# Optimization experiments

Measured on AMD Instinct MI355X. Metric: run time of the kernel, lower is better.

## Reference

```python
import jax, jax.numpy as jnp
import numpy as np

NUM_HEADS = 16
HEAD_DIM = 64
D_DEC = 1024
D_ENC = 1024
R = 256  # kv_lora_rank
LN_EPS = 1e-5


def setup_inputs() -> dict:
    key = jax.random.key(0)
    ks = jax.random.split(key, 8)
    B, SQ, SK = 4, 2048, 4096
    query = jax.random.normal(ks[0], (B, SQ, D_DEC), dtype=jnp.float32)
    encoder_output = jax.random.normal(ks[1], (B, SK, D_ENC), dtype=jnp.float32)
    s = 0.02
    Wq = jax.random.normal(ks[2], (NUM_HEADS * HEAD_DIM, D_DEC), dtype=jnp.float32) * s
    Wkva = jax.random.normal(ks[3], (R, D_ENC), dtype=jnp.float32) * s
    ln_g = jnp.ones((R,), dtype=jnp.float32)
    ln_b = jnp.zeros((R,), dtype=jnp.float32)
    Wkvb = jax.random.normal(ks[4], (NUM_HEADS * 2 * HEAD_DIM, R), dtype=jnp.float32) * s
    Wout = jax.random.normal(ks[5], (D_DEC, NUM_HEADS * HEAD_DIM), dtype=jnp.float32) * s
    return {"query": query, "encoder_output": encoder_output, "Wq": Wq,
            "Wkva": Wkva, "ln_g": ln_g, "ln_b": ln_b, "Wkvb": Wkvb, "Wout": Wout}


def reference(query, encoder_output, Wq, Wkva, ln_g, ln_b, Wkvb, Wout):
    B, SQ, _ = query.shape
    SK = encoder_output.shape[1]
    H, Dh = NUM_HEADS, HEAD_DIM

    # q projection -> [B, H, SQ, Dh]
    q = jnp.einsum('bsd,ed->bse', query, Wq).reshape(B, SQ, H, Dh).transpose(0, 2, 1, 3)

    # low-rank KV compression + layernorm
    c = jnp.einsum('bsd,rd->bsr', encoder_output, Wkva)  # [B, SK, R]
    mu = jnp.mean(c, axis=-1, keepdims=True)
    var = jnp.mean(jnp.square(c - mu), axis=-1, keepdims=True)
    c = (c - mu) * jax.lax.rsqrt(var + LN_EPS) * ln_g + ln_b

    # decompress to K,V: [B, SK, H, 2*Dh] -> split
    kv = jnp.einsum('bsr,er->bse', c, Wkvb).reshape(B, SK, H, 2 * Dh).transpose(0, 2, 1, 3)
    k, v = kv[..., :Dh], kv[..., Dh:]

    scale = 1.0 / np.sqrt(Dh).astype(np.float32)
    scores = jnp.einsum('bhqd,bhkd->bhqk', q, k) * scale
    attn = jax.nn.softmax(scores, axis=-1)  # dropout is identity in eval / p=0
    o = jnp.einsum('bhqk,bhkd->bhqd', attn, v)
    o = o.transpose(0, 2, 1, 3).reshape(B, SQ, H * Dh)
    return jnp.einsum('bse,de->bsd', o, Wout)
```

## Files before the change

kernel.cpp:

```cpp
#include <hip/hip_runtime.h>

#define LOG2E 1.4426950408889634f

typedef __attribute__((ext_vector_type(8))) short short8;
typedef __attribute__((ext_vector_type(4))) float f32x4;

__device__ inline unsigned short f2bf(float f) {
  unsigned u = __float_as_uint(f);
  u += 0x7fffu + ((u >> 16) & 1u);
  return (unsigned short)(u >> 16);
}

#define MFMA16(a, b, c) __builtin_amdgcn_mfma_f32_16x16x32_bf16((a), (b), (c), 0, 0, 0)

#define GLDS16(gp, lp)                                                              \
  __builtin_amdgcn_global_load_lds((const __attribute__((address_space(1))) void*)(gp), \
                                   (__attribute__((address_space(3))) void*)(lp), 16, 0, 0)

__device__ inline f32x4 zero4() {
  f32x4 z = {0.f, 0.f, 0.f, 0.f};
  return z;
}

__device__ inline int swz8(int row) { return (row ^ (row >> 3)) & 7; }

__global__ __launch_bounds__(256) void k_cast6(
    const float* __restrict__ e, const float* __restrict__ q, const float* __restrict__ wq,
    const float* __restrict__ wo, const float* __restrict__ wb, const float* __restrict__ wa,
    unsigned short* __restrict__ eo, unsigned short* __restrict__ qo, unsigned short* __restrict__ wqo,
    unsigned short* __restrict__ woo, unsigned short* __restrict__ wbo, unsigned short* __restrict__ wao) {
  int i = (blockIdx.x * 256 + threadIdx.x) * 4;
  const float* src;
  unsigned short* dst;
  int off;
  if (i < 16777216) { src = e; dst = eo; off = i; }
  else if (i < 25165824) { src = q; dst = qo; off = i - 16777216; }
  else if (i < 26214400) { src = wq; dst = wqo; off = i - 25165824; }
  else if (i < 27262976) { src = wo; dst = woo; off = i - 26214400; }
  else if (i < 27787264) { src = wb; dst = wbo; off = i - 27262976; }
  else { src = wa; dst = wao; off = i - 27787264; }
  float4 v = *(const float4*)(src + off);
  unsigned lo = (unsigned)f2bf(v.x) | ((unsigned)f2bf(v.y) << 16);
  unsigned hi = (unsigned)f2bf(v.z) | ((unsigned)f2bf(v.w) << 16);
  *(uint2*)(dst + off) = make_uint2(lo, hi);
}

__global__ __launch_bounds__(256, 2) void k_qproj(const unsigned short* __restrict__ A,
                                                  const unsigned short* __restrict__ Bw,
                                                  unsigned short* __restrict__ Qout) {
  __shared__ __align__(16) short As[128 * 32];
  __shared__ __align__(16) short Bs[128 * 32];
  const int K = 1024;
  int tid = threadIdx.x;
  int w = tid >> 6, lane = tid & 63, quad = lane >> 4, c = lane & 15;
  int m0 = blockIdx.x * 128, n0 = blockIdx.y * 128;
  int wm = (w >> 1) * 64, wn = (w & 1) * 64;
  f32x4 acc[4][4];
#pragma unroll
  for (int i = 0; i < 4; i++)
#pragma unroll
    for (int j = 0; j < 4; j++) acc[i][j] = zero4();

  for (int k0 = 0; k0 < K; k0 += 32) {
#pragma unroll
    for (int i = 0; i < 2; i++) {
      int seg = w * 2 + i;
      int bo = seg * 1024 + lane * 16;
      int row = bo >> 6, col = (bo & 63) >> 1;
      GLDS16(A + (size_t)(m0 + row) * K + k0 + col, (char*)As + seg * 1024);
      GLDS16(Bw + (size_t)(n0 + row) * K + k0 + col, (char*)Bs + seg * 1024);
    }
    __syncthreads();
    short8 af[4], bfr[4];
#pragma unroll
    for (int i = 0; i < 4; i++) {
      af[i] = *(const short8*)&As[(wm + i * 16 + c) * 32 + quad * 8];
      bfr[i] = *(const short8*)&Bs[(wn + i * 16 + c) * 32 + quad * 8];
    }
#pragma unroll
    for (int mi = 0; mi < 4; mi++)
#pragma unroll
      for (int ni = 0; ni < 4; ni++) acc[mi][ni] = MFMA16(af[mi], bfr[ni], acc[mi][ni]);
    __syncthreads();
  }
  const float scale = 0.125f * LOG2E;
#pragma unroll
  for (int mi = 0; mi < 4; mi++) {
    int rowb = m0 + wm + mi * 16 + quad * 4;
#pragma unroll
    for (int ni = 0; ni < 4; ni++) {
      int col = n0 + wn + ni * 16 + c;
      int h = col >> 6, d = col & 63;
#pragma unroll
      for (int r = 0; r < 4; r++) {
        int row = rowb + r;
        int b = row >> 11, sq = row & 2047;
        Qout[(((size_t)(b * 16 + h)) * 2048 + sq) * 64 + d] = f2bf(acc[mi][ni][r] * scale);
      }
    }
  }
}

__global__ __launch_bounds__(256, 2) void k_cln(const unsigned short* __restrict__ E,
                                                const unsigned short* __restrict__ Wa,
                                                const float* __restrict__ g, const float* __restrict__ bb,
                                                unsigned short* __restrict__ Cout) {
  __shared__ __align__(16) short As[64 * 32];
  __shared__ __align__(16) short Bs[256 * 32];
  __shared__ float redS[4][64], redQ[4][64];
  __shared__ float gS[256], bS[256];
  const int K = 1024;
  int tid = threadIdx.x;
  int w = tid >> 6, lane = tid & 63, quad = lane >> 4, c = lane & 15;
  int m0 = blockIdx.x * 64;
  gS[tid] = g[tid];
  bS[tid] = bb[tid];
  f32x4 acc[4][4];
#pragma unroll
  for (int i = 0; i < 4; i++)
#pragma unroll
    for (int j = 0; j < 4; j++) acc[i][j] = zero4();

  for (int k0 = 0; k0 < K; k0 += 32) {
    {
      int bo = w * 1024 + lane * 16;
      int row = bo >> 6, col = (bo & 63) >> 1;
      GLDS16(E + (size_t)(m0 + row) * K + k0 + col, (char*)As + w * 1024);
    }
#pragma unroll
    for (int i = 0; i < 4; i++) {
      int seg = w * 4 + i;
      int bo = seg * 1024 + lane * 16;
      int row = bo >> 6, col = (bo & 63) >> 1;
      GLDS16(Wa + (size_t)row * K + k0 + col, (char*)Bs + seg * 1024);
    }
    __syncthreads();
    short8 af[4], bfr[4];
#pragma unroll
    for (int i = 0; i < 4; i++) {
      af[i] = *(const short8*)&As[(i * 16 + c) * 32 + quad * 8];
      bfr[i] = *(const short8*)&Bs[(w * 64 + i * 16 + c) * 32 + quad * 8];
    }
#pragma unroll
    for (int mi = 0; mi < 4; mi++)
#pragma unroll
      for (int ni = 0; ni < 4; ni++) acc[mi][ni] = MFMA16(af[mi], bfr[ni], acc[mi][ni]);
    __syncthreads();
  }
  float ps[4][4], pq[4][4];
#pragma unroll
  for (int mi = 0; mi < 4; mi++)
#pragma unroll
    for (int r = 0; r < 4; r++) {
      float s = 0.f, q = 0.f;
#pragma unroll
      for (int ni = 0; ni < 4; ni++) {
        float x = acc[mi][ni][r];
        s += x;
        q += x * x;
      }
      for (int m = 1; m < 16; m <<= 1) {
        s += __shfl_xor(s, m, 64);
        q += __shfl_xor(q, m, 64);
      }
      ps[mi][r] = s;
      pq[mi][r] = q;
    }
  if (c == 0) {
#pragma unroll
    for (int mi = 0; mi < 4; mi++)
#pragma unroll
      for (int r = 0; r < 4; r++) {
        int row = mi * 16 + quad * 4 + r;
        redS[w][row] = ps[mi][r];
        redQ[w][row] = pq[mi][r];
      }
  }
  __syncthreads();
  float muv[4][4], rsv[4][4];
#pragma unroll
  for (int mi = 0; mi < 4; mi++)
#pragma unroll
    for (int r = 0; r < 4; r++) {
      int row = mi * 16 + quad * 4 + r;
      float S = redS[0][row] + redS[1][row] + redS[2][row] + redS[3][row];
      float Q = redQ[0][row] + redQ[1][row] + redQ[2][row] + redQ[3][row];
      float mu = S * (1.f / 256.f);
      float var = Q * (1.f / 256.f) - mu * mu;
      muv[mi][r] = mu;
      rsv[mi][r] = rsqrtf(var + 1e-5f);
    }
#pragma unroll
  for (int mi = 0; mi < 4; mi++)
#pragma unroll
    for (int ni = 0; ni < 4; ni++) {
      int col = w * 64 + ni * 16 + c;
#pragma unroll
      for (int r = 0; r < 4; r++) {
        int row = m0 + mi * 16 + quad * 4 + r;
        float y = (acc[mi][ni][r] - muv[mi][r]) * rsv[mi][r] * gS[col] + bS[col];
        Cout[(size_t)row * 256 + col] = f2bf(y);
      }
    }
}

__global__ __launch_bounds__(256, 2) void k_kv(const unsigned short* __restrict__ A,
                                               const unsigned short* __restrict__ Bw,
                                               unsigned short* __restrict__ Kb,
                                               unsigned short* __restrict__ Vb) {
  __shared__ __align__(16) short As[128 * 32];
  __shared__ __align__(16) short Bs[128 * 32];
  const int K = 256;
  int tid = threadIdx.x;
  int w = tid >> 6, lane = tid & 63, quad = lane >> 4, c = lane & 15;
  int m0 = blockIdx.x * 128, n0 = blockIdx.y * 128;
  int wm = (w >> 1) * 64, wn = (w & 1) * 64;
  f32x4 acc[4][4];
#pragma unroll
  for (int i = 0; i < 4; i++)
#pragma unroll
    for (int j = 0; j < 4; j++) acc[i][j] = zero4();

  for (int k0 = 0; k0 < K; k0 += 32) {
#pragma unroll
    for (int i = 0; i < 2; i++) {
      int seg = w * 2 + i;
      int bo = seg * 1024 + lane * 16;
      int row = bo >> 6, col = (bo & 63) >> 1;
      GLDS16(A + (size_t)(m0 + row) * K + k0 + col, (char*)As + seg * 1024);
      GLDS16(Bw + (size_t)(n0 + row) * K + k0 + col, (char*)Bs + seg * 1024);
    }
    __syncthreads();
    short8 af[4], bfr[4];
#pragma unroll
    for (int i = 0; i < 4; i++) {
      af[i] = *(const short8*)&As[(wm + i * 16 + c) * 32 + quad * 8];
      bfr[i] = *(const short8*)&Bs[(wn + i * 16 + c) * 32 + quad * 8];
    }
#pragma unroll
    for (int mi = 0; mi < 4; mi++)
#pragma unroll
      for (int ni = 0; ni < 4; ni++) acc[mi][ni] = MFMA16(af[mi], bfr[ni], acc[mi][ni]);
    __syncthreads();
  }
#pragma unroll
  for (int mi = 0; mi < 4; mi++) {
    int rowb = m0 + wm + mi * 16 + quad * 4;
#pragma unroll
    for (int ni = 0; ni < 4; ni++) {
      int col = n0 + wn + ni * 16 + c;
      int h = col >> 7, rr = col & 127;
#pragma unroll
      for (int r = 0; r < 4; r++) {
        int row = rowb + r;
        int b = row >> 12, sk = row & 4095;
        float x = acc[mi][ni][r];
        if (rr < 64)
          Kb[(((size_t)(b * 16 + h)) * 4096 + sk) * 64 + rr] = f2bf(x);
        else
          Vb[(((size_t)(b * 16 + h)) * 64 + (rr - 64)) * 4096 + sk] = f2bf(x);
      }
    }
  }
}

__global__ __launch_bounds__(256, 2) void k_attn(const unsigned short* __restrict__ Qb,
                                                 const unsigned short* __restrict__ Kb,
                                                 const unsigned short* __restrict__ Vb,
                                                 unsigned short* __restrict__ Ob) {
  __shared__ __align__(16) short Qs[256 * 64];
  __shared__ __align__(16) short KVs[2][2 * 64 * 64];
  int tid = threadIdx.x;
  int w = tid >> 6, lane = tid & 63, quad = lane >> 4, c = lane & 15;
  int r8 = lane >> 3, pc = lane & 7;
  int bh = blockIdx.y, qt = blockIdx.x;
  const unsigned short* Qp = Qb + ((size_t)bh * 2048 + qt * 256) * 64;
  const unsigned short* Kp = Kb + (size_t)bh * 4096 * 64;
  const unsigned short* Vp = Vb + (size_t)bh * 64 * 4096;

#pragma unroll
  for (int i = 0; i < 8; i++) {
    int seg = w * 8 + i;
    int row = seg * 8 + r8;
    int lc = pc ^ swz8(row);
    GLDS16(Qp + (size_t)row * 64 + lc * 8, (char*)Qs + seg * 1024);
  }
#pragma unroll
  for (int i = 0; i < 4; i++) {
    int seg = w * 4 + i;
    int row = (seg & 7) * 8 + r8;
    int lc = pc ^ swz8(row);
    if (seg < 8)
      GLDS16(Kp + (size_t)row * 64 + lc * 8, (char*)KVs[0] + seg * 1024);
    else
      GLDS16(Vp + (size_t)row * 4096 + lc * 8, (char*)KVs[0] + seg * 1024);
  }
  __syncthreads();
  short8 qf[4][2];
#pragma unroll
  for (int nt = 0; nt < 4; nt++) {
    int row = w * 64 + nt * 16 + c;
#pragma unroll
    for (int kk = 0; kk < 2; kk++)
      qf[nt][kk] = *(const short8*)((const char*)Qs + row * 128 + (((kk * 4 + quad) ^ swz8(row)) << 4));
  }
  char* PsW = (char*)Qs + w * 8192;

  f32x4 O[4][4];
  float lp[4] = {0.f, 0.f, 0.f, 0.f};
#pragma unroll
  for (int i = 0; i < 4; i++)
#pragma unroll
    for (int j = 0; j < 4; j++) O[i][j] = zero4();

  for (int kt = 0; kt < 64; kt++) {
    const char* KsC = (const char*)KVs[kt & 1];
    const char* VsC = KsC + 8192;
    if (kt < 63) {
      char* nb = (char*)KVs[(kt + 1) & 1];
#pragma unroll
      for (int i = 0; i < 4; i++) {
        int seg = w * 4 + i;
        int row = (seg & 7) * 8 + r8;
        int lc = pc ^ swz8(row);
        if (seg < 8)
          GLDS16(Kp + ((size_t)(kt + 1) * 64 + row) * 64 + lc * 8, nb + seg * 1024);
        else
          GLDS16(Vp + (size_t)row * 4096 + (kt + 1) * 64 + lc * 8, nb + seg * 1024);
      }
    }

#pragma unroll
    for (int mt = 0; mt < 4; mt++) {
      int krow = mt * 16 + c;
      short8 kf0 = *(const short8*)(KsC + krow * 128 + ((quad ^ swz8(krow)) << 4));
      short8 kf1 = *(const short8*)(KsC + krow * 128 + (((4 + quad) ^ swz8(krow)) << 4));
      f32x4 s[4];
#pragma unroll
      for (int nt = 0; nt < 4; nt++) {
        s[nt] = MFMA16(kf0, qf[nt][0], zero4());
        s[nt] = MFMA16(kf1, qf[nt][1], s[nt]);
      }
#pragma unroll
      for (int nt = 0; nt < 4; nt++) {
        float p0 = __builtin_amdgcn_exp2f(s[nt][0]);
        float p1 = __builtin_amdgcn_exp2f(s[nt][1]);
        float p2 = __builtin_amdgcn_exp2f(s[nt][2]);
        float p3 = __builtin_amdgcn_exp2f(s[nt][3]);
        lp[nt] += (p0 + p1) + (p2 + p3);
        unsigned u0 = ((__float_as_uint(p0) + 0x8000u) >> 16) | ((__float_as_uint(p1) + 0x8000u) & 0xffff0000u);
        unsigned u1 = ((__float_as_uint(p2) + 0x8000u) >> 16) | ((__float_as_uint(p3) + 0x8000u) & 0xffff0000u);
        int prow = nt * 16 + c;
        int chunk = (mt * 2 + (quad >> 1)) ^ swz8(prow);
        *(uint2*)(PsW + prow * 128 + (chunk << 4) + (quad & 1) * 8) = make_uint2(u0, u1);
      }
    }

#pragma unroll
    for (int kk = 0; kk < 2; kk++) {
      short8 vf[4];
#pragma unroll
      for (int dt = 0; dt < 4; dt++) {
        int vrow = dt * 16 + c;
        vf[dt] = *(const short8*)(VsC + vrow * 128 + (((kk * 4 + quad) ^ swz8(vrow)) << 4));
      }
#pragma unroll
      for (int mo = 0; mo < 4; mo++) {
        int prow = mo * 16 + c;
        short8 pf = *(const short8*)((const char*)PsW + prow * 128 + (((kk * 4 + quad) ^ swz8(prow)) << 4));
#pragma unroll
        for (int dt = 0; dt < 4; dt++) O[mo][dt] = MFMA16(pf, vf[dt], O[mo][dt]);
      }
    }
    __syncthreads();
  }

#pragma unroll
  for (int nt = 0; nt < 4; nt++) {
    lp[nt] += __shfl_xor(lp[nt], 16, 64);
    lp[nt] += __shfl_xor(lp[nt], 32, 64);
  }
  int b = bh >> 4, h = bh & 15;
#pragma unroll
  for (int mo = 0; mo < 4; mo++) {
#pragma unroll
    for (int r = 0; r < 4; r++) {
      float inv = __builtin_amdgcn_rcpf(__shfl(lp[mo], quad * 4 + r, 64));
      int sq = qt * 256 + w * 64 + mo * 16 + quad * 4 + r;
#pragma unroll
      for (int dt = 0; dt < 4; dt++)
        Ob[((size_t)b * 2048 + sq) * 1024 + h * 64 + dt * 16 + c] = f2bf(O[mo][dt][r] * inv);
    }
  }
}

__global__ __launch_bounds__(256, 2) void k_out(const unsigned short* __restrict__ A,
                                                const unsigned short* __restrict__ Bw,
                                                float* __restrict__ Out) {
  __shared__ __align__(16) short As[128 * 32];
  __shared__ __align__(16) short Bs[128 * 32];
  const int K = 1024;
  int tid = threadIdx.x;
  int w = tid >> 6, lane = tid & 63, quad = lane >> 4, c = lane & 15;
  int m0 = blockIdx.x * 128, n0 = blockIdx.y * 128;
  int wm = (w >> 1) * 64, wn = (w & 1) * 64;
  f32x4 acc[4][4];
#pragma unroll
  for (int i = 0; i < 4; i++)
#pragma unroll
    for (int j = 0; j < 4; j++) acc[i][j] = zero4();

  for (int k0 = 0; k0 < K; k0 += 32) {
#pragma unroll
    for (int i = 0; i < 2; i++) {
      int seg = w * 2 + i;
      int bo = seg * 1024 + lane * 16;
      int row = bo >> 6, col = (bo & 63) >> 1;
      GLDS16(A + (size_t)(m0 + row) * K + k0 + col, (char*)As + seg * 1024);
      GLDS16(Bw + (size_t)(n0 + row) * K + k0 + col, (char*)Bs + seg * 1024);
    }
    __syncthreads();
    short8 af[4], bfr[4];
#pragma unroll
    for (int i = 0; i < 4; i++) {
      af[i] = *(const short8*)&As[(wm + i * 16 + c) * 32 + quad * 8];
      bfr[i] = *(const short8*)&Bs[(wn + i * 16 + c) * 32 + quad * 8];
    }
#pragma unroll
    for (int mi = 0; mi < 4; mi++)
#pragma unroll
      for (int ni = 0; ni < 4; ni++) acc[mi][ni] = MFMA16(af[mi], bfr[ni], acc[mi][ni]);
    __syncthreads();
  }
#pragma unroll
  for (int mi = 0; mi < 4; mi++) {
    int rowb = m0 + wm + mi * 16 + quad * 4;
#pragma unroll
    for (int ni = 0; ni < 4; ni++) {
      int col = n0 + wn + ni * 16 + c;
#pragma unroll
      for (int r = 0; r < 4; r++) Out[(size_t)(rowb + r) * 1024 + col] = acc[mi][ni][r];
    }
  }
}

extern "C" void kernel_launch(void* const* d_in, const int* in_sizes, int n_in,
                              void* d_out, int out_size, void* d_ws, size_t ws_size,
                              hipStream_t stream) {
  const float* query = (const float*)d_in[0];
  const float* enc = (const float*)d_in[1];
  const float* Wq = (const float*)d_in[2];
  const float* Wkva = (const float*)d_in[3];
  const float* ln_g = (const float*)d_in[4];
  const float* ln_b = (const float*)d_in[5];
  const float* Wkvb = (const float*)d_in[6];
  const float* Wout = (const float*)d_in[7];
  if (ws_size < 81264640) return;

  char* ws = (char*)d_ws;
  unsigned short* wq_bf = (unsigned short*)(ws + 0);
  unsigned short* wa_bf = (unsigned short*)(ws + 2097152);
  unsigned short* wb_bf = (unsigned short*)(ws + 2621440);
  unsigned short* wo_bf = (unsigned short*)(ws + 3670016);
  unsigned short* qproj = (unsigned short*)(ws + 5767168);
  unsigned short* cln = (unsigned short*)(ws + 22544384);
  unsigned short* ebf_v = (unsigned short*)(ws + 30932992);
  unsigned short* qin_o = (unsigned short*)(ws + 64487424);
  unsigned short* kbuf = (unsigned short*)d_out;

  k_cast6<<<27392, 256, 0, stream>>>(enc, query, Wq, Wout, Wkvb, Wkva,
                                     ebf_v, qin_o, wq_bf, wo_bf, wb_bf, wa_bf);

  k_qproj<<<dim3(64, 8), 256, 0, stream>>>(qin_o, wq_bf, qproj);
  k_cln<<<256, 256, 0, stream>>>(ebf_v, wa_bf, ln_g, ln_b, cln);
  k_kv<<<dim3(128, 16), 256, 0, stream>>>(cln, wb_bf, kbuf, ebf_v);
  k_attn<<<dim3(8, 64), 256, 0, stream>>>(qproj, kbuf, ebf_v, qin_o);
  k_out<<<dim3(64, 8), 256, 0, stream>>>(qin_o, wo_bf, (float*)d_out);
}
```

Baseline: 460.7 us.

## Split attention over key halves with combine kernel and single-buffered LDS

The attention kernel is templated to split the key sequence into NS chunks across a new grid dimension. Each chunk writes unnormalized bf16 partial outputs and row sums, and a new k_comb kernel adds the partials and normalizes them. The split path runs only when the workspace is large enough. Q fragments are now loaded straight from global memory into registers, and KV staging drops to a single LDS buffer with a per-wave P tile, which reduces LDS use so launch bounds can target 4 blocks per CU. The aim is more blocks per CU and more parallelism (1024 blocks instead of 512), at the cost of an extra pass over the output, lost overlap of the next KV load with compute, and extra bf16 rounding of the partials.

```diff
diff --git a/kernel.cpp b/kernel.cpp
--- a/kernel.cpp
+++ b/kernel.cpp
@@ -264,47 +264,56 @@
   }
 }
 
-__global__ __launch_bounds__(256, 2) void k_attn(const unsigned short* __restrict__ Qb,
+template <int NS>
+__global__ __launch_bounds__(256, 4) void k_attn(const unsigned short* __restrict__ Qb,
                                                  const unsigned short* __restrict__ Kb,
                                                  const unsigned short* __restrict__ Vb,
-                                                 unsigned short* __restrict__ Ob) {
-  __shared__ __align__(16) short Qs[256 * 64];
-  __shared__ __align__(16) short KVs[2][2 * 64 * 64];
+                                                 unsigned short* __restrict__ O0,
+                                                 unsigned short* __restrict__ O1,
+                                                 float* __restrict__ l0,
+                                                 float* __restrict__ l1) {
+  __shared__ __align__(16) short KVs[2 * 64 * 64];
+  __shared__ __align__(16) short Ps[4][2048];
   int tid = threadIdx.x;
   int w = tid >> 6, lane = tid & 63, quad = lane >> 4, c = lane & 15;
   int r8 = lane >> 3, pc = lane & 7;
-  int bh = blockIdx.y, qt = blockIdx.x;
-  const unsigned short* Qp = Qb + ((size_t)bh * 2048 + qt * 256) * 64;
-  const unsigned short* Kp = Kb + (size_t)bh * 4096 * 64;
-  const unsigned short* Vp = Vb + (size_t)bh * 64 * 4096;
-
-#pragma unroll
-  for (int i = 0; i < 8; i++) {
-    int seg = w * 8 + i;
-    int row = seg * 8 + r8;
-    int lc = pc ^ swz8(row);
-    GLDS16(Qp + (size_t)row * 64 + lc * 8, (char*)Qs + seg * 1024);
-  }
+  int qt = blockIdx.x, ks = blockIdx.y, bh = blockIdx.z;
+  const int ITERS = 64 / NS;
+
+  const char* Kg = (const char*)Kb + (size_t)bh * 524288 + (size_t)ks * 262144;
+  const char* Vg = (const char*)Vb + (size_t)bh * 524288 + (size_t)ks * 4096;
+  const unsigned short* Qv = Qb + ((size_t)bh * 2048 + qt * 256 + w * 64) * 64 + c * 64 + quad * 8;
+
+  const char* sg[4];
+  int step = (w < 2) ? 8192 : 128;
 #pragma unroll
   for (int i = 0; i < 4; i++) {
     int seg = w * 4 + i;
-    int row = (seg & 7) * 8 + r8;
-    int lc = pc ^ swz8(row);
-    if (seg < 8)
-      GLDS16(Kp + (size_t)row * 64 + lc * 8, (char*)KVs[0] + seg * 1024);
-    else
-      GLDS16(Vp + (size_t)row * 4096 + lc * 8, (char*)KVs[0] + seg * 1024);
-  }
-  __syncthreads();
+    if (w < 2) {
+      int row = seg * 8 + r8;
+      sg[i] = Kg + row * 128 + ((pc ^ r8) << 4);
+    } else {
+      int vrow = (seg - 8) * 8 + r8;
+      sg[i] = Vg + (size_t)vrow * 8192 + ((pc ^ r8) << 4);
+    }
+  }
+
+  int kb0 = c * 128 + ((quad ^ (c & 7)) << 4);
+  int kb1 = c * 128 + (((quad + 4) ^ (c & 7)) << 4);
+  const char* KsB0 = (const char*)KVs + kb0;
+  const char* KsB1 = (const char*)KVs + kb1;
+  const char* VsB0 = (const char*)KVs + 8192 + kb0;
+  const char* VsB1 = (const char*)KVs + 8192 + kb1;
+  int sP = (c >> 1) & 3;
+  char* pw0 = (char*)Ps[w] + c * 64 + (quad & 1) * 8 + (((quad >> 1) ^ sP) << 4);
+  char* pw1 = (char*)Ps[w] + c * 64 + (quad & 1) * 8 + ((((quad >> 1) + 2) ^ sP) << 4);
+  const char* prB = (const char*)Ps[w] + c * 64 + ((quad ^ sP) << 4);
+
   short8 qf[4][2];
 #pragma unroll
-  for (int nt = 0; nt < 4; nt++) {
-    int row = w * 64 + nt * 16 + c;
-#pragma unroll
-    for (int kk = 0; kk < 2; kk++)
-      qf[nt][kk] = *(const short8*)((const char*)Qs + row * 128 + (((kk * 4 + quad) ^ swz8(row)) << 4));
-  }
-  char* PsW = (char*)Qs + w * 8192;
+  for (int nt = 0; nt < 4; nt++)
+#pragma unroll
+    for (int h = 0; h < 2; h++) qf[nt][h] = *(const short8*)(Qv + nt * 1024 + h * 32);
 
   f32x4 O[4][4];
   float lp[4] = {0.f, 0.f, 0.f, 0.f};
@@ -313,66 +322,64 @@
 #pragma unroll
     for (int j = 0; j < 4; j++) O[i][j] = zero4();
 
-  for (int kt = 0; kt < 64; kt++) {
-    const char* KsC = (const char*)KVs[kt & 1];
-    const char* VsC = KsC + 8192;
-    if (kt < 63) {
-      char* nb = (char*)KVs[(kt + 1) & 1];
+#pragma unroll
+  for (int i = 0; i < 4; i++) {
+    GLDS16(sg[i], (char*)KVs + (w * 4 + i) * 1024);
+    sg[i] += step;
+  }
+
+  for (int kt = 0; kt < ITERS; kt++) {
+    __syncthreads();
+#pragma unroll
+    for (int kk = 0; kk < 2; kk++) {
+#pragma unroll
+      for (int mtl = 0; mtl < 2; mtl++) {
+        int mt = kk * 2 + mtl;
+        short8 kf0 = *(const short8*)(KsB0 + mt * 2048);
+        short8 kf1 = *(const short8*)(KsB1 + mt * 2048);
+        f32x4 s[4];
+#pragma unroll
+        for (int nt = 0; nt < 4; nt++) {
+          s[nt] = MFMA16(kf0, qf[nt][0], zero4());
+          s[nt] = MFMA16(kf1, qf[nt][1], s[nt]);
+        }
+#pragma unroll
+        for (int nt = 0; nt < 4; nt++) {
+          float p0 = __builtin_amdgcn_exp2f(s[nt][0]);
+          float p1 = __builtin_amdgcn_exp2f(s[nt][1]);
+          float p2 = __builtin_amdgcn_exp2f(s[nt][2]);
+          float p3 = __builtin_amdgcn_exp2f(s[nt][3]);
+          lp[nt] += (p0 + p1) + (p2 + p3);
+          unsigned r0 = __float_as_uint(p0) + 0x8000u;
+          unsigned r1 = __float_as_uint(p1) + 0x8000u;
+          unsigned r2 = __float_as_uint(p2) + 0x8000u;
+          unsigned r3 = __float_as_uint(p3) + 0x8000u;
+          unsigned lo = __builtin_amdgcn_perm(r1, r0, 0x07060302u);
+          unsigned hi = __builtin_amdgcn_perm(r3, r2, 0x07060302u);
+          *(uint2*)((mtl ? pw1 : pw0) + nt * 1024) = make_uint2(lo, hi);
+        }
+      }
+      {
+        const char* VsB = kk ? VsB1 : VsB0;
+        short8 vf[4];
+#pragma unroll
+        for (int dt = 0; dt < 4; dt++) vf[dt] = *(const short8*)(VsB + dt * 2048);
+#pragma unroll
+        for (int mo = 0; mo < 4; mo++) {
+          short8 pf = *(const short8*)(prB + mo * 1024);
+#pragma unroll
+          for (int dt = 0; dt < 4; dt++) O[mo][dt] = MFMA16(pf, vf[dt], O[mo][dt]);
+        }
+      }
+    }
+    __syncthreads();
+    if (kt + 1 < ITERS) {
 #pragma unroll
       for (int i = 0; i < 4; i++) {
-        int seg = w * 4 + i;
-        int row = (seg & 7) * 8 + r8;
-        int lc = pc ^ swz8(row);
-        if (seg < 8)
-          GLDS16(Kp + ((size_t)(kt + 1) * 64 + row) * 64 + lc * 8, nb + seg * 1024);
-        else
-          GLDS16(Vp + (size_t)row * 4096 + (kt + 1) * 64 + lc * 8, nb + seg * 1024);
-      }
-    }
-
-#pragma unroll
-    for (int mt = 0; mt < 4; mt++) {
-      int krow = mt * 16 + c;
-      short8 kf0 = *(const short8*)(KsC + krow * 128 + ((quad ^ swz8(krow)) << 4));
-      short8 kf1 = *(const short8*)(KsC + krow * 128 + (((4 + quad) ^ swz8(krow)) << 4));
-      f32x4 s[4];
-#pragma unroll
-      for (int nt = 0; nt < 4; nt++) {
-        s[nt] = MFMA16(kf0, qf[nt][0], zero4());
-        s[nt] = MFMA16(kf1, qf[nt][1], s[nt]);
-      }
-#pragma unroll
-      for (int nt = 0; nt < 4; nt++) {
-        float p0 = __builtin_amdgcn_exp2f(s[nt][0]);
-        float p1 = __builtin_amdgcn_exp2f(s[nt][1]);
-        float p2 = __builtin_amdgcn_exp2f(s[nt][2]);
-        float p3 = __builtin_amdgcn_exp2f(s[nt][3]);
-        lp[nt] += (p0 + p1) + (p2 + p3);
-        unsigned u0 = ((__float_as_uint(p0) + 0x8000u) >> 16) | ((__float_as_uint(p1) + 0x8000u) & 0xffff0000u);
-        unsigned u1 = ((__float_as_uint(p2) + 0x8000u) >> 16) | ((__float_as_uint(p3) + 0x8000u) & 0xffff0000u);
-        int prow = nt * 16 + c;
-        int chunk = (mt * 2 + (quad >> 1)) ^ swz8(prow);
-        *(uint2*)(PsW + prow * 128 + (chunk << 4) + (quad & 1) * 8) = make_uint2(u0, u1);
-      }
-    }
-
-#pragma unroll
-    for (int kk = 0; kk < 2; kk++) {
-      short8 vf[4];
-#pragma unroll
-      for (int dt = 0; dt < 4; dt++) {
-        int vrow = dt * 16 + c;
-        vf[dt] = *(const short8*)(VsC + vrow * 128 + (((kk * 4 + quad) ^ swz8(vrow)) << 4));
-      }
-#pragma unroll
-      for (int mo = 0; mo < 4; mo++) {
-        int prow = mo * 16 + c;
-        short8 pf = *(const short8*)((const char*)PsW + prow * 128 + (((kk * 4 + quad) ^ swz8(prow)) << 4));
-#pragma unroll
-        for (int dt = 0; dt < 4; dt++) O[mo][dt] = MFMA16(pf, vf[dt], O[mo][dt]);
-      }
-    }
-    __syncthreads();
+        GLDS16(sg[i], (char*)KVs + (w * 4 + i) * 1024);
+        sg[i] += step;
+      }
+    }
   }
 
 #pragma unroll
@@ -381,17 +388,57 @@
     lp[nt] += __shfl_xor(lp[nt], 32, 64);
   }
   int b = bh >> 4, h = bh & 15;
-#pragma unroll
-  for (int mo = 0; mo < 4; mo++) {
-#pragma unroll
-    for (int r = 0; r < 4; r++) {
-      float inv = __builtin_amdgcn_rcpf(__shfl(lp[mo], quad * 4 + r, 64));
-      int sq = qt * 256 + w * 64 + mo * 16 + quad * 4 + r;
-#pragma unroll
-      for (int dt = 0; dt < 4; dt++)
-        Ob[((size_t)b * 2048 + sq) * 1024 + h * 64 + dt * 16 + c] = f2bf(O[mo][dt][r] * inv);
-    }
-  }
+  if (NS == 1) {
+#pragma unroll
+    for (int mo = 0; mo < 4; mo++) {
+#pragma unroll
+      for (int r = 0; r < 4; r++) {
+        float inv = __builtin_amdgcn_rcpf(__shfl(lp[mo], quad * 4 + r, 64));
+        int sq = qt * 256 + w * 64 + mo * 16 + quad * 4 + r;
+#pragma unroll
+        for (int dt = 0; dt < 4; dt++)
+          O0[((size_t)b * 2048 + sq) * 1024 + h * 64 + dt * 16 + c] = f2bf(O[mo][dt][r] * inv);
+      }
+    }
+  } else {
+    unsigned short* Op = ks ? O1 : O0;
+    float* lq = ks ? l1 : l0;
+#pragma unroll
+    for (int mo = 0; mo < 4; mo++) {
+#pragma unroll
+      for (int r = 0; r < 4; r++) {
+        int sq = qt * 256 + w * 64 + mo * 16 + quad * 4 + r;
+#pragma unroll
+        for (int dt = 0; dt < 4; dt++)
+          Op[((size_t)b * 2048 + sq) * 1024 + h * 64 + dt * 16 + c] = f2bf(O[mo][dt][r]);
+      }
+    }
+    float lsel = lp[0];
+    if (quad == 1) lsel = lp[1];
+    if (quad == 2) lsel = lp[2];
+    if (quad == 3) lsel = lp[3];
+    lq[(size_t)bh * 2048 + qt * 256 + w * 64 + quad * 16 + c] = lsel;
+  }
+}
+
+__global__ __launch_bounds__(256) void k_comb(unsigned short* __restrict__ A,
+                                              const unsigned short* __restrict__ Bp,
+                                              const float* __restrict__ lA,
+                                              const float* __restrict__ lB) {
+  int i = (blockIdx.x * 256 + threadIdx.x) * 4;
+  int row = i >> 10, col = i & 1023;
+  int bh = ((row >> 11) << 4) + (col >> 6);
+  int li = bh * 2048 + (row & 2047);
+  float inv = __builtin_amdgcn_rcpf(lA[li] + lB[li]);
+  uint2 a = *(const uint2*)(A + i);
+  uint2 bb = *(const uint2*)(Bp + i);
+  float o0 = __uint_as_float(a.x << 16) + __uint_as_float(bb.x << 16);
+  float o1 = __uint_as_float(a.x & 0xffff0000u) + __uint_as_float(bb.x & 0xffff0000u);
+  float o2 = __uint_as_float(a.y << 16) + __uint_as_float(bb.y << 16);
+  float o3 = __uint_as_float(a.y & 0xffff0000u) + __uint_as_float(bb.y & 0xffff0000u);
+  unsigned lo = (unsigned)f2bf(o0 * inv) | ((unsigned)f2bf(o1 * inv) << 16);
+  unsigned hi = (unsigned)f2bf(o2 * inv) | ((unsigned)f2bf(o3 * inv) << 16);
+  *(uint2*)(A + i) = make_uint2(lo, hi);
 }
 
 __global__ __launch_bounds__(256, 2) void k_out(const unsigned short* __restrict__ A,
@@ -458,22 +505,49 @@
   if (ws_size < 81264640) return;
 
   char* ws = (char*)d_ws;
-  unsigned short* wq_bf = (unsigned short*)(ws + 0);
-  unsigned short* wa_bf = (unsigned short*)(ws + 2097152);
-  unsigned short* wb_bf = (unsigned short*)(ws + 2621440);
-  unsigned short* wo_bf = (unsigned short*)(ws + 3670016);
-  unsigned short* qproj = (unsigned short*)(ws + 5767168);
-  unsigned short* cln = (unsigned short*)(ws + 22544384);
-  unsigned short* ebf_v = (unsigned short*)(ws + 30932992);
-  unsigned short* qin_o = (unsigned short*)(ws + 64487424);
+  bool split = ws_size >= 87031808;
+
+  unsigned short *qbf, *ebf_v, *qproj, *cln, *oA, *oB, *wq_bf, *wa_bf, *wb_bf, *wo_bf;
+  float *lA, *lB;
+  if (split) {
+    qbf = (unsigned short*)(ws + 0);
+    ebf_v = (unsigned short*)(ws + 16777216);
+    qproj = (unsigned short*)(ws + 50331648);
+    oB = (unsigned short*)(ws + 67108864);
+    cln = (unsigned short*)(ws + 67108864);
+    wq_bf = (unsigned short*)(ws + 75497472);
+    wa_bf = (unsigned short*)(ws + 77594624);
+    wb_bf = (unsigned short*)(ws + 78118912);
+    lA = (float*)(ws + 83886080);
+    lB = (float*)(ws + 84410368);
+    wo_bf = (unsigned short*)(ws + 84934656);
+    oA = qbf;
+  } else {
+    wq_bf = (unsigned short*)(ws + 0);
+    wa_bf = (unsigned short*)(ws + 2097152);
+    wb_bf = (unsigned short*)(ws + 2621440);
+    wo_bf = (unsigned short*)(ws + 3670016);
+    qproj = (unsigned short*)(ws + 5767168);
+    cln = (unsigned short*)(ws + 22544384);
+    ebf_v = (unsigned short*)(ws + 30932992);
+    qbf = (unsigned short*)(ws + 64487424);
+    oA = qbf;
+    oB = qbf;
+    lA = lB = (float*)(ws + 22544384);
+  }
   unsigned short* kbuf = (unsigned short*)d_out;
 
   k_cast6<<<27392, 256, 0, stream>>>(enc, query, Wq, Wout, Wkvb, Wkva,
-                                     ebf_v, qin_o, wq_bf, wo_bf, wb_bf, wa_bf);
-
-  k_qproj<<<dim3(64, 8), 256, 0, stream>>>(qin_o, wq_bf, qproj);
+                                     ebf_v, qbf, wq_bf, wo_bf, wb_bf, wa_bf);
+
+  k_qproj<<<dim3(64, 8), 256, 0, stream>>>(qbf, wq_bf, qproj);
   k_cln<<<256, 256, 0, stream>>>(ebf_v, wa_bf, ln_g, ln_b, cln);
   k_kv<<<dim3(128, 16), 256, 0, stream>>>(cln, wb_bf, kbuf, ebf_v);
-  k_attn<<<dim3(8, 64), 256, 0, stream>>>(qproj, kbuf, ebf_v, qin_o);
-  k_out<<<dim3(64, 8), 256, 0, stream>>>(qin_o, wo_bf, (float*)d_out);
-}
+  if (split) {
+    k_attn<2><<<dim3(8, 2, 64), 256, 0, stream>>>(qproj, kbuf, ebf_v, oA, oB, lA, lB);
+    k_comb<<<16384, 256, 0, stream>>>(oA, oB, lA, lB);
+  } else {
+    k_attn<1><<<dim3(8, 1, 64), 256, 0, stream>>>(qproj, kbuf, ebf_v, oA, oB, lA, lB);
+  }
+  k_out<<<dim3(64, 8), 256, 0, stream>>>(oA, wo_bf, (float*)d_out);
+}
```

After: 671.0 us. 1.46x slower.

## Shrink attention query tile to 128 rows and single-buffer KV for occupancy

Applied to the files above, without the earlier changes.

The attention kernel now processes 128 query rows per block (32 per wave) instead of 256, launching twice as many blocks with launch bounds raised to 4 blocks per CU. KV shared memory goes from double-buffered to a single buffer with barriers on both sides of each tile. Q fragments are loaded straight from global into registers instead of being staged in LDS, and swizzle addresses are precomputed outside the loop. The goal is higher occupancy and less per-iteration address arithmetic. The cost is that K/V loads no longer overlap compute within a block, so overlap has to come from other resident blocks, and each K/V tile is reloaded by twice as many blocks.

```diff
diff --git a/kernel.cpp b/kernel.cpp
--- a/kernel.cpp
+++ b/kernel.cpp
@@ -21,8 +21,6 @@
   f32x4 z = {0.f, 0.f, 0.f, 0.f};
   return z;
 }
-
-__device__ inline int swz8(int row) { return (row ^ (row >> 3)) & 7; }
 
 __global__ __launch_bounds__(256) void k_cast6(
     const float* __restrict__ e, const float* __restrict__ q, const float* __restrict__ wq,
@@ -264,129 +262,131 @@
   }
 }
 
-__global__ __launch_bounds__(256, 2) void k_attn(const unsigned short* __restrict__ Qb,
+__global__ __launch_bounds__(256, 4) void k_attn(const unsigned short* __restrict__ Qb,
                                                  const unsigned short* __restrict__ Kb,
                                                  const unsigned short* __restrict__ Vb,
                                                  unsigned short* __restrict__ Ob) {
-  __shared__ __align__(16) short Qs[256 * 64];
-  __shared__ __align__(16) short KVs[2][2 * 64 * 64];
+  __shared__ __align__(16) short KVs[2 * 64 * 64];
+  __shared__ __align__(16) short Ps[4][2048];
   int tid = threadIdx.x;
   int w = tid >> 6, lane = tid & 63, quad = lane >> 4, c = lane & 15;
   int r8 = lane >> 3, pc = lane & 7;
-  int bh = blockIdx.y, qt = blockIdx.x;
-  const unsigned short* Qp = Qb + ((size_t)bh * 2048 + qt * 256) * 64;
-  const unsigned short* Kp = Kb + (size_t)bh * 4096 * 64;
-  const unsigned short* Vp = Vb + (size_t)bh * 64 * 4096;
-
-#pragma unroll
-  for (int i = 0; i < 8; i++) {
-    int seg = w * 8 + i;
-    int row = seg * 8 + r8;
-    int lc = pc ^ swz8(row);
-    GLDS16(Qp + (size_t)row * 64 + lc * 8, (char*)Qs + seg * 1024);
-  }
+  int qt = blockIdx.x, bh = blockIdx.y;
+
+  const char* Kg = (const char*)Kb + (size_t)bh * 524288;
+  const char* Vg = (const char*)Vb + (size_t)bh * 524288;
+  const unsigned short* Qv = Qb + ((size_t)bh * 2048 + qt * 128 + w * 32) * 64 + c * 64 + quad * 8;
+
+  const char* sg[4];
+  int step = (w < 2) ? 8192 : 128;
 #pragma unroll
   for (int i = 0; i < 4; i++) {
     int seg = w * 4 + i;
-    int row = (seg & 7) * 8 + r8;
-    int lc = pc ^ swz8(row);
-    if (seg < 8)
-      GLDS16(Kp + (size_t)row * 64 + lc * 8, (char*)KVs[0] + seg * 1024);
-    else
-      GLDS16(Vp + (size_t)row * 4096 + lc * 8, (char*)KVs[0] + seg * 1024);
-  }
-  __syncthreads();
-  short8 qf[4][2];
-#pragma unroll
-  for (int nt = 0; nt < 4; nt++) {
-    int row = w * 64 + nt * 16 + c;
-#pragma unroll
-    for (int kk = 0; kk < 2; kk++)
-      qf[nt][kk] = *(const short8*)((const char*)Qs + row * 128 + (((kk * 4 + quad) ^ swz8(row)) << 4));
-  }
-  char* PsW = (char*)Qs + w * 8192;
-
-  f32x4 O[4][4];
-  float lp[4] = {0.f, 0.f, 0.f, 0.f};
-#pragma unroll
-  for (int i = 0; i < 4; i++)
+    if (w < 2) {
+      int row = seg * 8 + r8;
+      sg[i] = Kg + row * 128 + ((pc ^ r8) << 4);
+    } else {
+      int vrow = (seg - 8) * 8 + r8;
+      sg[i] = Vg + (size_t)vrow * 8192 + ((pc ^ r8) << 4);
+    }
+  }
+
+  int c7 = c & 7;
+  int kb0 = c * 128 + ((quad ^ c7) << 4);
+  int kb1 = c * 128 + (((quad + 4) ^ c7) << 4);
+  const char* KsB0 = (const char*)KVs + kb0;
+  const char* KsB1 = (const char*)KVs + kb1;
+  const char* VsB0 = (const char*)KVs + 8192 + kb0;
+  const char* VsB1 = (const char*)KVs + 8192 + kb1;
+  char* pwm[4];
+#pragma unroll
+  for (int mt = 0; mt < 4; mt++)
+    pwm[mt] = (char*)Ps[w] + c * 128 + (quad & 1) * 8 + ((((mt * 2) ^ (quad >> 1) ^ c7)) << 4);
+  const char* pr0 = (const char*)Ps[w] + c * 128 + ((quad ^ c7) << 4);
+  const char* pr1 = (const char*)Ps[w] + c * 128 + (((quad + 4) ^ c7) << 4);
+
+  short8 qf[2][2];
+#pragma unroll
+  for (int nt = 0; nt < 2; nt++)
+#pragma unroll
+    for (int h = 0; h < 2; h++) qf[nt][h] = *(const short8*)(Qv + nt * 1024 + h * 32);
+
+  f32x4 O[2][4];
+  float lp[2] = {0.f, 0.f};
+#pragma unroll
+  for (int i = 0; i < 2; i++)
 #pragma unroll
     for (int j = 0; j < 4; j++) O[i][j] = zero4();
 
+#pragma unroll
+  for (int i = 0; i < 4; i++) {
+    GLDS16(sg[i], (char*)KVs + (w * 4 + i) * 1024);
+    sg[i] += step;
+  }
+
   for (int kt = 0; kt < 64; kt++) {
-    const char* KsC = (const char*)KVs[kt & 1];
-    const char* VsC = KsC + 8192;
+    __syncthreads();
+#pragma unroll
+    for (int mt = 0; mt < 4; mt++) {
+      short8 kf0 = *(const short8*)(KsB0 + mt * 2048);
+      short8 kf1 = *(const short8*)(KsB1 + mt * 2048);
+      f32x4 s0 = MFMA16(kf0, qf[0][0], zero4());
+      s0 = MFMA16(kf1, qf[0][1], s0);
+      f32x4 s1 = MFMA16(kf0, qf[1][0], zero4());
+      s1 = MFMA16(kf1, qf[1][1], s1);
+#pragma unroll
+      for (int nt = 0; nt < 2; nt++) {
+        f32x4 s = nt ? s1 : s0;
+        float p0 = __builtin_amdgcn_exp2f(s[0]);
+        float p1 = __builtin_amdgcn_exp2f(s[1]);
+        float p2 = __builtin_amdgcn_exp2f(s[2]);
+        float p3 = __builtin_amdgcn_exp2f(s[3]);
+        lp[nt] += (p0 + p1) + (p2 + p3);
+        unsigned r0 = __float_as_uint(p0) + 0x8000u;
+        unsigned r1 = __float_as_uint(p1) + 0x8000u;
+        unsigned r2 = __float_as_uint(p2) + 0x8000u;
+        unsigned r3 = __float_as_uint(p3) + 0x8000u;
+        unsigned lo = __builtin_amdgcn_perm(r1, r0, 0x07060302u);
+        unsigned hi = __builtin_amdgcn_perm(r3, r2, 0x07060302u);
+        *(uint2*)(pwm[mt] + nt * 2048) = make_uint2(lo, hi);
+      }
+    }
+#pragma unroll
+    for (int kk = 0; kk < 2; kk++) {
+      const char* VsB = kk ? VsB1 : VsB0;
+      const char* pr = kk ? pr1 : pr0;
+      short8 vf[4];
+#pragma unroll
+      for (int dt = 0; dt < 4; dt++) vf[dt] = *(const short8*)(VsB + dt * 2048);
+#pragma unroll
+      for (int mo = 0; mo < 2; mo++) {
+        short8 pf = *(const short8*)(pr + mo * 2048);
+#pragma unroll
+        for (int dt = 0; dt < 4; dt++) O[mo][dt] = MFMA16(pf, vf[dt], O[mo][dt]);
+      }
+    }
+    __syncthreads();
     if (kt < 63) {
-      char* nb = (char*)KVs[(kt + 1) & 1];
 #pragma unroll
       for (int i = 0; i < 4; i++) {
-        int seg = w * 4 + i;
-        int row = (seg & 7) * 8 + r8;
-        int lc = pc ^ swz8(row);
-        if (seg < 8)
-          GLDS16(Kp + ((size_t)(kt + 1) * 64 + row) * 64 + lc * 8, nb + seg * 1024);
-        else
-          GLDS16(Vp + (size_t)row * 4096 + (kt + 1) * 64 + lc * 8, nb + seg * 1024);
-      }
-    }
-
-#pragma unroll
-    for (int mt = 0; mt < 4; mt++) {
-      int krow = mt * 16 + c;
-      short8 kf0 = *(const short8*)(KsC + krow * 128 + ((quad ^ swz8(krow)) << 4));
-      short8 kf1 = *(const short8*)(KsC + krow * 128 + (((4 + quad) ^ swz8(krow)) << 4));
-      f32x4 s[4];
-#pragma unroll
-      for (int nt = 0; nt < 4; nt++) {
-        s[nt] = MFMA16(kf0, qf[nt][0], zero4());
-        s[nt] = MFMA16(kf1, qf[nt][1], s[nt]);
-      }
-#pragma unroll
-      for (int nt = 0; nt < 4; nt++) {
-        float p0 = __builtin_amdgcn_exp2f(s[nt][0]);
-        float p1 = __builtin_amdgcn_exp2f(s[nt][1]);
-        float p2 = __builtin_amdgcn_exp2f(s[nt][2]);
-        float p3 = __builtin_amdgcn_exp2f(s[nt][3]);
-        lp[nt] += (p0 + p1) + (p2 + p3);
-        unsigned u0 = ((__float_as_uint(p0) + 0x8000u) >> 16) | ((__float_as_uint(p1) + 0x8000u) & 0xffff0000u);
-        unsigned u1 = ((__float_as_uint(p2) + 0x8000u) >> 16) | ((__float_as_uint(p3) + 0x8000u) & 0xffff0000u);
-        int prow = nt * 16 + c;
-        int chunk = (mt * 2 + (quad >> 1)) ^ swz8(prow);
-        *(uint2*)(PsW + prow * 128 + (chunk << 4) + (quad & 1) * 8) = make_uint2(u0, u1);
-      }
-    }
-
-#pragma unroll
-    for (int kk = 0; kk < 2; kk++) {
-      short8 vf[4];
-#pragma unroll
-      for (int dt = 0; dt < 4; dt++) {
-        int vrow = dt * 16 + c;
-        vf[dt] = *(const short8*)(VsC + vrow * 128 + (((kk * 4 + quad) ^ swz8(vrow)) << 4));
-      }
-#pragma unroll
-      for (int mo = 0; mo < 4; mo++) {
-        int prow = mo * 16 + c;
-        short8 pf = *(const short8*)((const char*)PsW + prow * 128 + (((kk * 4 + quad) ^ swz8(prow)) << 4));
-#pragma unroll
-        for (int dt = 0; dt < 4; dt++) O[mo][dt] = MFMA16(pf, vf[dt], O[mo][dt]);
-      }
-    }
-    __syncthreads();
-  }
-
-#pragma unroll
-  for (int nt = 0; nt < 4; nt++) {
+        GLDS16(sg[i], (char*)KVs + (w * 4 + i) * 1024);
+        sg[i] += step;
+      }
+    }
+  }
+
+#pragma unroll
+  for (int nt = 0; nt < 2; nt++) {
     lp[nt] += __shfl_xor(lp[nt], 16, 64);
     lp[nt] += __shfl_xor(lp[nt], 32, 64);
   }
   int b = bh >> 4, h = bh & 15;
 #pragma unroll
-  for (int mo = 0; mo < 4; mo++) {
+  for (int mo = 0; mo < 2; mo++) {
 #pragma unroll
     for (int r = 0; r < 4; r++) {
       float inv = __builtin_amdgcn_rcpf(__shfl(lp[mo], quad * 4 + r, 64));
-      int sq = qt * 256 + w * 64 + mo * 16 + quad * 4 + r;
+      int sq = qt * 128 + w * 32 + mo * 16 + quad * 4 + r;
 #pragma unroll
       for (int dt = 0; dt < 4; dt++)
         Ob[((size_t)b * 2048 + sq) * 1024 + h * 64 + dt * 16 + c] = f2bf(O[mo][dt][r] * inv);
@@ -474,6 +474,6 @@
   k_qproj<<<dim3(64, 8), 256, 0, stream>>>(qin_o, wq_bf, qproj);
   k_cln<<<256, 256, 0, stream>>>(ebf_v, wa_bf, ln_g, ln_b, cln);
   k_kv<<<dim3(128, 16), 256, 0, stream>>>(cln, wb_bf, kbuf, ebf_v);
-  k_attn<<<dim3(8, 64), 256, 0, stream>>>(qproj, kbuf, ebf_v, qin_o);
+  k_attn<<<dim3(16, 64), 256, 0, stream>>>(qproj, kbuf, ebf_v, qin_o);
   k_out<<<dim3(64, 8), 256, 0, stream>>>(qin_o, wo_bf, (float*)d_out);
 }
```

Result: faster. 441.6 us (-4.1%).
